# Optimization experiments

Measured on AMD Instinct MI355X. Metric: run time of the kernel, lower is better.

The kernel has to match this reference:

```python
import jax, jax.numpy as jnp
import numpy as np

B, S, D = 4, 4096, 2048
E, H, SPE = 64, 1024, 1
NUM_SLOTS = E * SPE
TEMP = 1.0


def setup_inputs() -> dict:
    key = jax.random.key(0)
    ks = jax.random.split(key, 6)
    x = jax.random.normal(ks[0], (B, S, D), dtype=jnp.float32)
    W_disp = jax.random.normal(ks[1], (NUM_SLOTS, D), dtype=jnp.float32) * 0.02
    # torch Linear default init ~ U(-1/sqrt(fan_in), 1/sqrt(fan_in))
    W1 = jax.random.uniform(ks[2], (E, H, D), jnp.float32, -1.0, 1.0) / np.sqrt(D)
    b1 = jax.random.uniform(ks[3], (E, H), jnp.float32, -1.0, 1.0) / np.sqrt(D)
    W2 = jax.random.uniform(ks[4], (E, D, H), jnp.float32, -1.0, 1.0) / np.sqrt(H)
    b2 = jax.random.uniform(ks[5], (E, D), jnp.float32, -1.0, 1.0) / np.sqrt(H)
    return {"x": x, "W_disp": W_disp, "W1": W1, "b1": b1, "W2": W2, "b2": b2}


def reference(x, W_disp, W1, b1, W2, b2):
    # eval mode: dropout inactive, no calibration, z_loss_weight=0
    Bb, Ss, Dd = x.shape
    xf = x.reshape(-1, Dd)                       # (T, D)
    logits = (xf @ W_disp.T) / TEMP              # (T, num_slots)
    dispatch = jax.nn.softmax(logits, axis=0)    # softmax over tokens (T > 1)
    combine = jax.nn.softmax(logits, axis=-1)    # softmax over slots
    slot_inputs = dispatch.T @ xf                # (num_slots, D)
    x_exp = slot_inputs.reshape(E, SPE, Dd)      # (E, S_per, D)
    h = jnp.einsum('esd,ehd->esh', x_exp, W1) + b1[:, None, :]
    h = jax.nn.gelu(h, approximate=False)        # torch F.gelu is exact (erf)
    out = jnp.einsum('esh,edh->esd', h, W2) + b2[:, None, :]
    slot_outputs = out.reshape(NUM_SLOTS, Dd)
    y = combine @ slot_outputs                   # (T, D)
    return y.reshape(Bb, Ss, Dd)
```

## Files before the change

kernel.cpp:

```cpp
#include <hip/hip_runtime.h>
#include <math.h>

#define T_TOK 16384
#define D_DIM 2048
#define NSLOT 64
#define H_DIM 1024
#define KSPLIT 8
#define KCH (D_DIM / KSPLIT)

__global__ __launch_bounds__(256) void k_logits(const float* __restrict__ x,
                                                const float* __restrict__ Wd,
                                                float* __restrict__ plog) {
    __shared__ float xs[256][32];
    __shared__ float ws[64][32];
    const int tid = threadIdx.x;
    const int tblk = blockIdx.x * 256;
    const int ks = blockIdx.y;
    const int koff = ks * KCH;
    const int tq = tid >> 3;
    const int sg = tid & 7;
    float acc[8][8] = {};

    for (int kc = 0; kc < KCH; kc += 32) {
        __syncthreads();
        #pragma unroll
        for (int ii = 0; ii < 8; ++ii) {
            int fi = tid + ii * 256;
            int t = fi >> 3, c = fi & 7;
            *(float4*)&xs[t][(c ^ (t & 7)) << 2] =
                *(const float4*)&x[(size_t)(tblk + t) * D_DIM + koff + kc + c * 4];
        }
        #pragma unroll
        for (int ii = 0; ii < 2; ++ii) {
            int fi = tid + ii * 256;
            int s = fi >> 3, c = fi & 7;
            *(float4*)&ws[s][(c ^ (s & 7)) << 2] =
                *(const float4*)&Wd[(size_t)s * D_DIM + koff + kc + c * 4];
        }
        __syncthreads();
        #pragma unroll
        for (int c = 0; c < 8; ++c) {
            float4 wv[8];
            #pragma unroll
            for (int j = 0; j < 8; ++j)
                wv[j] = *(const float4*)&ws[sg + 8 * j][(c ^ sg) << 2];
            #pragma unroll
            for (int i = 0; i < 8; ++i) {
                float4 xv = *(const float4*)&xs[tq + 32 * i][(c ^ (tq & 7)) << 2];
                #pragma unroll
                for (int j = 0; j < 8; ++j)
                    acc[i][j] += xv.x * wv[j].x + xv.y * wv[j].y +
                                 xv.z * wv[j].z + xv.w * wv[j].w;
            }
        }
    }
    #pragma unroll
    for (int i = 0; i < 8; ++i)
        #pragma unroll
        for (int j = 0; j < 8; ++j)
            plog[((size_t)ks * T_TOK + tblk + tq + 32 * i) * NSLOT + sg + 8 * j] =
                acc[i][j];
}

__global__ __launch_bounds__(256) void k_lsum(const float* __restrict__ plog,
                                              float* __restrict__ logits) {
    const size_t idx = ((size_t)blockIdx.x * 256 + threadIdx.x) * 4;
    float4 a = *(const float4*)&plog[idx];
    #pragma unroll
    for (int j = 1; j < KSPLIT; ++j) {
        float4 v = *(const float4*)&plog[(size_t)j * T_TOK * NSLOT + idx];
        a.x += v.x; a.y += v.y; a.z += v.z; a.w += v.w;
    }
    *(float4*)&logits[idx] = a;
}

__global__ __launch_bounds__(256) void k_cred1(const float* __restrict__ logits,
                                               float* __restrict__ pm,
                                               float* __restrict__ pz) {
    __shared__ float lm[256], lz[256];
    const int tid = threadIdx.x;
    const size_t base = (size_t)blockIdx.x * 256 * NSLOT;
    float m = -1e30f, z = 0.f;
    for (int i = 0; i < 64; ++i) {
        float v = logits[base + (size_t)i * 256 + tid];
        float nm = fmaxf(m, v);
        z = z * __expf(m - nm) + __expf(v - nm);
        m = nm;
    }
    lm[tid] = m; lz[tid] = z;
    __syncthreads();
    if (tid < 64) {
        float M = lm[tid], Z = lz[tid];
        #pragma unroll
        for (int i = 1; i < 4; ++i) {
            float m2 = lm[tid + i * 64], z2 = lz[tid + i * 64];
            float nm = fmaxf(M, m2);
            Z = Z * __expf(M - nm) + z2 * __expf(m2 - nm);
            M = nm;
        }
        pm[blockIdx.x * NSLOT + tid] = M;
        pz[blockIdx.x * NSLOT + tid] = Z;
    }
}

__global__ void k_cred2(const float* __restrict__ pm, const float* __restrict__ pz,
                        float* __restrict__ m_out, float* __restrict__ invZ_out) {
    const int s = threadIdx.x;
    float M = -1e30f, Z = 0.f;
    for (int i = 0; i < 64; ++i) {
        float m2 = pm[i * NSLOT + s], z2 = pz[i * NSLOT + s];
        float nm = fmaxf(M, m2);
        Z = Z * __expf(M - nm) + z2 * __expf(m2 - nm);
        M = nm;
    }
    m_out[s] = M;
    invZ_out[s] = 1.f / Z;
}

__global__ __launch_bounds__(256) void k_probs(const float* __restrict__ logits,
                                               const float* __restrict__ mS,
                                               const float* __restrict__ invZ,
                                               float* __restrict__ disp,
                                               float* __restrict__ comb) {
    const int wave = threadIdx.x >> 6, lane = threadIdx.x & 63;
    const int t = blockIdx.x * 4 + wave;
    float v = logits[(size_t)t * NSLOT + lane];
    float M = v;
    #pragma unroll
    for (int off = 32; off; off >>= 1) M = fmaxf(M, __shfl_xor(M, off));
    float e = __expf(v - M);
    float Z = e;
    #pragma unroll
    for (int off = 32; off; off >>= 1) Z += __shfl_xor(Z, off);
    comb[(size_t)t * NSLOT + lane] = e / Z;
    disp[(size_t)t * NSLOT + lane] = __expf(v - mS[lane]) * invZ[lane];
}

__global__ __launch_bounds__(256) void k_slot_inputs(const float* __restrict__ x,
        const float* __restrict__ disp, float* __restrict__ partial) {
    __shared__ float xs[32][256];
    __shared__ float pls[32][64];
    const int tid = threadIdx.x;
    const int d0 = blockIdx.x * 256;
    const int tc0 = blockIdx.y * 256;
    const int dg = tid & 31;
    const int sgq = tid >> 5;
    float4 acc0[8] = {}, acc1[8] = {};

    for (int sub = 0; sub < 8; ++sub) {
        const int t0 = tc0 + sub * 32;
        __syncthreads();
        #pragma unroll
        for (int ii = 0; ii < 8; ++ii) {
            int fi = tid + ii * 256;
            int r = fi >> 6, c4 = fi & 63;
            *(float4*)&xs[r][c4 * 4] =
                *(const float4*)&x[(size_t)(t0 + r) * D_DIM + d0 + c4 * 4];
        }
        #pragma unroll
        for (int ii = 0; ii < 2; ++ii) {
            int fi = tid + ii * 256;
            int r = fi >> 4, s4 = fi & 15;
            *(float4*)&pls[r][s4 * 4] =
                *(const float4*)&disp[(size_t)(t0 + r) * NSLOT + s4 * 4];
        }
        __syncthreads();
        for (int t = 0; t < 32; ++t) {
            float4 xv0 = *(const float4*)&xs[t][dg * 4];
            float4 xv1 = *(const float4*)&xs[t][128 + dg * 4];
            #pragma unroll
            for (int i = 0; i < 8; ++i) {
                float p = pls[t][sgq * 8 + i];
                acc0[i].x += p * xv0.x; acc0[i].y += p * xv0.y;
                acc0[i].z += p * xv0.z; acc0[i].w += p * xv0.w;
                acc1[i].x += p * xv1.x; acc1[i].y += p * xv1.y;
                acc1[i].z += p * xv1.z; acc1[i].w += p * xv1.w;
            }
        }
    }
    #pragma unroll
    for (int i = 0; i < 8; ++i) {
        int s = sgq * 8 + i;
        *(float4*)&partial[((size_t)blockIdx.y * NSLOT + s) * D_DIM + d0 + dg * 4] = acc0[i];
        *(float4*)&partial[((size_t)blockIdx.y * NSLOT + s) * D_DIM + d0 + 128 + dg * 4] = acc1[i];
    }
}

__global__ __launch_bounds__(256) void k_sred(const float* __restrict__ partial,
                                              float* __restrict__ slot_in) {
    const size_t idx = ((size_t)blockIdx.x * 256 + threadIdx.x) * 4;
    float4 a = {0.f, 0.f, 0.f, 0.f};
    for (int c = 0; c < 64; ++c) {
        float4 v = *(const float4*)&partial[(size_t)c * (NSLOT * D_DIM) + idx];
        a.x += v.x; a.y += v.y; a.z += v.z; a.w += v.w;
    }
    *(float4*)&slot_in[idx] = a;
}

__global__ __launch_bounds__(256) void k_mlp1(const float* __restrict__ W1,
                                              const float* __restrict__ b1,
                                              const float* __restrict__ slot_in,
                                              float* __restrict__ h) {
    const int wave = threadIdx.x >> 6, lane = threadIdx.x & 63;
    const int row = blockIdx.x * 4 + wave;
    const int e = row >> 10;
    const float* wr = W1 + (size_t)row * D_DIM;
    const float* xr = slot_in + (size_t)e * D_DIM;
    float acc = 0.f;
    #pragma unroll
    for (int i = 0; i < 8; ++i) {
        int k = (lane + i * 64) * 4;
        float4 w4 = *(const float4*)(wr + k);
        float4 x4 = *(const float4*)(xr + k);
        acc += w4.x * x4.x + w4.y * x4.y + w4.z * x4.z + w4.w * x4.w;
    }
    #pragma unroll
    for (int off = 32; off; off >>= 1) acc += __shfl_xor(acc, off);
    if (lane == 0) {
        float v = acc + b1[row];
        h[row] = 0.5f * v * (1.f + erff(v * 0.70710678118654752f));
    }
}

__global__ __launch_bounds__(256) void k_mlp2(const float* __restrict__ W2,
                                              const float* __restrict__ b2,
                                              const float* __restrict__ h,
                                              float* __restrict__ slot_out) {
    const int wave = threadIdx.x >> 6, lane = threadIdx.x & 63;
    const int row = blockIdx.x * 4 + wave;
    const int e = row >> 11;
    const float* wr = W2 + (size_t)row * H_DIM;
    const float* xr = h + (size_t)e * H_DIM;
    float acc = 0.f;
    #pragma unroll
    for (int i = 0; i < 4; ++i) {
        int k = (lane + i * 64) * 4;
        float4 w4 = *(const float4*)(wr + k);
        float4 x4 = *(const float4*)(xr + k);
        acc += w4.x * x4.x + w4.y * x4.y + w4.z * x4.z + w4.w * x4.w;
    }
    #pragma unroll
    for (int off = 32; off; off >>= 1) acc += __shfl_xor(acc, off);
    if (lane == 0) slot_out[row] = acc + b2[row];
}

__global__ __launch_bounds__(256) void k_combine(const float* __restrict__ comb,
                                                 const float* __restrict__ so,
                                                 float* __restrict__ y) {
    __shared__ float cl[128][68];
    __shared__ float sol[64][128];
    const int tid = threadIdx.x;
    const int d0 = blockIdx.x * 128;
    const int tb = blockIdx.y * 128;
    const int tq = tid >> 4;
    const int dgq = tid & 15;
    #pragma unroll
    for (int ii = 0; ii < 8; ++ii) {
        int fi = tid + ii * 256;
        int r = fi >> 4, s4 = fi & 15;
        *(float4*)&cl[r][s4 * 4] =
            *(const float4*)&comb[(size_t)(tb + r) * NSLOT + s4 * 4];
    }
    #pragma unroll
    for (int ii = 0; ii < 8; ++ii) {
        int fi = tid + ii * 256;
        int r = fi >> 5, c4 = fi & 31;
        *(float4*)&sol[r][c4 * 4] =
            *(const float4*)&so[(size_t)r * D_DIM + d0 + c4 * 4];
    }
    __syncthreads();
    float4 acc0[8] = {}, acc1[8] = {};
    for (int s = 0; s < 64; ++s) {
        float4 sv0 = *(const float4*)&sol[s][dgq * 4];
        float4 sv1 = *(const float4*)&sol[s][64 + dgq * 4];
        #pragma unroll
        for (int i = 0; i < 8; ++i) {
            float cv = cl[tq + 16 * i][s];
            acc0[i].x += cv * sv0.x; acc0[i].y += cv * sv0.y;
            acc0[i].z += cv * sv0.z; acc0[i].w += cv * sv0.w;
            acc1[i].x += cv * sv1.x; acc1[i].y += cv * sv1.y;
            acc1[i].z += cv * sv1.z; acc1[i].w += cv * sv1.w;
        }
    }
    #pragma unroll
    for (int i = 0; i < 8; ++i) {
        *(float4*)&y[(size_t)(tb + tq + 16 * i) * D_DIM + d0 + dgq * 4] = acc0[i];
        *(float4*)&y[(size_t)(tb + tq + 16 * i) * D_DIM + d0 + 64 + dgq * 4] = acc1[i];
    }
}

extern "C" void kernel_launch(void* const* d_in, const int* in_sizes, int n_in,
                              void* d_out, int out_size, void* d_ws, size_t ws_size,
                              hipStream_t stream) {
    const float* x  = (const float*)d_in[0];
    const float* Wd = (const float*)d_in[1];
    const float* W1 = (const float*)d_in[2];
    const float* b1 = (const float*)d_in[3];
    const float* W2 = (const float*)d_in[4];
    const float* b2 = (const float*)d_in[5];
    float* y = (float*)d_out;

    float* w = (float*)d_ws;
    float* plog    = w;
    float* logits  = plog + (size_t)KSPLIT * T_TOK * NSLOT;
    float* pm      = logits + (size_t)T_TOK * NSLOT;
    float* pz      = pm + 64 * NSLOT;
    float* mS      = pz + 64 * NSLOT;
    float* invZ    = mS + NSLOT;
    float* disp    = invZ + NSLOT;
    float* comb    = disp + (size_t)T_TOK * NSLOT;
    float* partial = comb + (size_t)T_TOK * NSLOT;
    float* slot_in = partial + (size_t)64 * NSLOT * D_DIM;
    float* h       = slot_in + (size_t)NSLOT * D_DIM;
    float* slot_out= h + (size_t)NSLOT * H_DIM;

    k_logits<<<dim3(T_TOK / 256, KSPLIT), 256, 0, stream>>>(x, Wd, plog);
    k_lsum<<<(T_TOK * NSLOT) / (4 * 256), 256, 0, stream>>>(plog, logits);
    k_cred1<<<64, 256, 0, stream>>>(logits, pm, pz);
    k_cred2<<<1, 64, 0, stream>>>(pm, pz, mS, invZ);
    k_probs<<<T_TOK / 4, 256, 0, stream>>>(logits, mS, invZ, disp, comb);
    k_slot_inputs<<<dim3(8, 64), 256, 0, stream>>>(x, disp, partial);
    k_sred<<<(NSLOT * D_DIM) / (4 * 256), 256, 0, stream>>>(partial, slot_in);
    k_mlp1<<<(NSLOT * H_DIM) / 4, 256, 0, stream>>>(W1, b1, slot_in, h);
    k_mlp2<<<(NSLOT * D_DIM) / 4, 256, 0, stream>>>(W2, b2, h, slot_out);
    k_combine<<<dim3(16, 128), 256, 0, stream>>>(comb, slot_out, y);
}
```

Measured before the change: 509.5 us.

## Fuse router front-end stages into one cooperative persistent kernel with grid syncs

Replaces seven front-end launches (logits GEMM, split-K sum, column softmax reductions, probs, slot-input GEMM, slot reduction) with a single cooperative kernel of 256 blocks separated by grid.sync. It halves KSPLIT, fuses the logit sum with per-block column stats and the row softmax, and computes dispatch probabilities on the fly instead of storing them. The aim is to cut launch gaps and intermediate global traffic. In exchange it runs far fewer blocks per stage (256 vs up to 512), pays for grid barriers, and serializes the final stat merge on one block.

```diff
diff --git a/kernel.cpp b/kernel.cpp
--- a/kernel.cpp
+++ b/kernel.cpp
@@ -1,200 +1,213 @@
 #include <hip/hip_runtime.h>
+#include <hip/hip_cooperative_groups.h>
 #include <math.h>
+
+namespace cg = cooperative_groups;
 
 #define T_TOK 16384
 #define D_DIM 2048
 #define NSLOT 64
 #define H_DIM 1024
-#define KSPLIT 8
-#define KCH (D_DIM / KSPLIT)
-
-__global__ __launch_bounds__(256) void k_logits(const float* __restrict__ x,
-                                                const float* __restrict__ Wd,
-                                                float* __restrict__ plog) {
-    __shared__ float xs[256][32];
-    __shared__ float ws[64][32];
+#define KSPLIT 4
+#define KCH 512
+#define NBLK 256
+
+__global__ __launch_bounds__(256, 2) void k_front(
+    const float* __restrict__ x, const float* __restrict__ Wd,
+    float* __restrict__ wsp)
+{
+    cg::grid_group grid = cg::this_grid();
     const int tid = threadIdx.x;
-    const int tblk = blockIdx.x * 256;
-    const int ks = blockIdx.y;
-    const int koff = ks * KCH;
-    const int tq = tid >> 3;
-    const int sg = tid & 7;
-    float acc[8][8] = {};
-
-    for (int kc = 0; kc < KCH; kc += 32) {
-        __syncthreads();
-        #pragma unroll
-        for (int ii = 0; ii < 8; ++ii) {
-            int fi = tid + ii * 256;
-            int t = fi >> 3, c = fi & 7;
-            *(float4*)&xs[t][(c ^ (t & 7)) << 2] =
-                *(const float4*)&x[(size_t)(tblk + t) * D_DIM + koff + kc + c * 4];
-        }
-        #pragma unroll
-        for (int ii = 0; ii < 2; ++ii) {
-            int fi = tid + ii * 256;
-            int s = fi >> 3, c = fi & 7;
-            *(float4*)&ws[s][(c ^ (s & 7)) << 2] =
-                *(const float4*)&Wd[(size_t)s * D_DIM + koff + kc + c * 4];
-        }
-        __syncthreads();
-        #pragma unroll
-        for (int c = 0; c < 8; ++c) {
-            float4 wv[8];
-            #pragma unroll
-            for (int j = 0; j < 8; ++j)
-                wv[j] = *(const float4*)&ws[sg + 8 * j][(c ^ sg) << 2];
-            #pragma unroll
-            for (int i = 0; i < 8; ++i) {
-                float4 xv = *(const float4*)&xs[tq + 32 * i][(c ^ (tq & 7)) << 2];
+    const int bid = blockIdx.x;
+
+    float* plog     = wsp;
+    float* logits   = plog + (size_t)KSPLIT * T_TOK * NSLOT;
+    float* comb     = logits + (size_t)T_TOK * NSLOT;
+    float* pm       = comb + (size_t)T_TOK * NSLOT;
+    float* pz       = pm + (size_t)NBLK * NSLOT;
+    float* mS       = pz + (size_t)NBLK * NSLOT;
+    float* invZ     = mS + NSLOT;
+    float* partial  = invZ + NSLOT;
+    float* slot_in  = partial + (size_t)32 * NSLOT * D_DIM;
+
+    __shared__ union {
+        struct { float xs[256][32]; float wsb[64][32]; } p1;
+        struct { float ls[64][66]; } p2;
+        struct { float lm[4][64]; float lz[4][64]; } p3;
+        struct { float xs[32][256]; float pls[32][64];
+                 float msh[64]; float zsh[64]; } p4;
+        struct { float4 red[256]; } p5;
+    } u;
+
+    {
+        const int tb = bid >> 2, ks = bid & 3;
+        const int tblk = tb * 256, koff = ks * KCH;
+        const int tq = tid >> 3, sg = tid & 7;
+        float acc[8][8] = {};
+        for (int kc = 0; kc < KCH; kc += 32) {
+            __syncthreads();
+            #pragma unroll
+            for (int ii = 0; ii < 8; ++ii) {
+                int fi = tid + ii * 256; int t = fi >> 3, c = fi & 7;
+                *(float4*)&u.p1.xs[t][(c ^ (t & 7)) << 2] =
+                    *(const float4*)&x[(size_t)(tblk + t) * D_DIM + koff + kc + c * 4];
+            }
+            #pragma unroll
+            for (int ii = 0; ii < 2; ++ii) {
+                int fi = tid + ii * 256; int s = fi >> 3, c = fi & 7;
+                *(float4*)&u.p1.wsb[s][(c ^ (s & 7)) << 2] =
+                    *(const float4*)&Wd[(size_t)s * D_DIM + koff + kc + c * 4];
+            }
+            __syncthreads();
+            #pragma unroll
+            for (int c = 0; c < 8; ++c) {
+                float4 wv[8];
                 #pragma unroll
                 for (int j = 0; j < 8; ++j)
-                    acc[i][j] += xv.x * wv[j].x + xv.y * wv[j].y +
-                                 xv.z * wv[j].z + xv.w * wv[j].w;
-            }
-        }
-    }
-    #pragma unroll
-    for (int i = 0; i < 8; ++i)
+                    wv[j] = *(const float4*)&u.p1.wsb[sg + 8 * j][(c ^ sg) << 2];
+                #pragma unroll
+                for (int i = 0; i < 8; ++i) {
+                    float4 xv = *(const float4*)&u.p1.xs[tq + 32 * i][(c ^ (tq & 7)) << 2];
+                    #pragma unroll
+                    for (int j = 0; j < 8; ++j)
+                        acc[i][j] += xv.x * wv[j].x + xv.y * wv[j].y +
+                                     xv.z * wv[j].z + xv.w * wv[j].w;
+                }
+            }
+        }
         #pragma unroll
-        for (int j = 0; j < 8; ++j)
-            plog[((size_t)ks * T_TOK + tblk + tq + 32 * i) * NSLOT + sg + 8 * j] =
-                acc[i][j];
-}
-
-__global__ __launch_bounds__(256) void k_lsum(const float* __restrict__ plog,
-                                              float* __restrict__ logits) {
-    const size_t idx = ((size_t)blockIdx.x * 256 + threadIdx.x) * 4;
-    float4 a = *(const float4*)&plog[idx];
-    #pragma unroll
-    for (int j = 1; j < KSPLIT; ++j) {
-        float4 v = *(const float4*)&plog[(size_t)j * T_TOK * NSLOT + idx];
-        a.x += v.x; a.y += v.y; a.z += v.z; a.w += v.w;
-    }
-    *(float4*)&logits[idx] = a;
-}
-
-__global__ __launch_bounds__(256) void k_cred1(const float* __restrict__ logits,
-                                               float* __restrict__ pm,
-                                               float* __restrict__ pz) {
-    __shared__ float lm[256], lz[256];
-    const int tid = threadIdx.x;
-    const size_t base = (size_t)blockIdx.x * 256 * NSLOT;
-    float m = -1e30f, z = 0.f;
-    for (int i = 0; i < 64; ++i) {
-        float v = logits[base + (size_t)i * 256 + tid];
-        float nm = fmaxf(m, v);
-        z = z * __expf(m - nm) + __expf(v - nm);
-        m = nm;
-    }
-    lm[tid] = m; lz[tid] = z;
-    __syncthreads();
-    if (tid < 64) {
-        float M = lm[tid], Z = lz[tid];
+        for (int i = 0; i < 8; ++i)
+            #pragma unroll
+            for (int j = 0; j < 8; ++j)
+                plog[((size_t)ks * T_TOK + tblk + tq + 32 * i) * NSLOT + sg + 8 * j] =
+                    acc[i][j];
+    }
+    grid.sync();
+
+    {
+        const int j0 = bid * 64;
         #pragma unroll
-        for (int i = 1; i < 4; ++i) {
-            float m2 = lm[tid + i * 64], z2 = lz[tid + i * 64];
-            float nm = fmaxf(M, m2);
-            Z = Z * __expf(M - nm) + z2 * __expf(m2 - nm);
-            M = nm;
-        }
-        pm[blockIdx.x * NSLOT + tid] = M;
-        pz[blockIdx.x * NSLOT + tid] = Z;
-    }
-}
-
-__global__ void k_cred2(const float* __restrict__ pm, const float* __restrict__ pz,
-                        float* __restrict__ m_out, float* __restrict__ invZ_out) {
-    const int s = threadIdx.x;
-    float M = -1e30f, Z = 0.f;
-    for (int i = 0; i < 64; ++i) {
-        float m2 = pm[i * NSLOT + s], z2 = pz[i * NSLOT + s];
-        float nm = fmaxf(M, m2);
-        Z = Z * __expf(M - nm) + z2 * __expf(m2 - nm);
-        M = nm;
-    }
-    m_out[s] = M;
-    invZ_out[s] = 1.f / Z;
-}
-
-__global__ __launch_bounds__(256) void k_probs(const float* __restrict__ logits,
-                                               const float* __restrict__ mS,
-                                               const float* __restrict__ invZ,
-                                               float* __restrict__ disp,
-                                               float* __restrict__ comb) {
-    const int wave = threadIdx.x >> 6, lane = threadIdx.x & 63;
-    const int t = blockIdx.x * 4 + wave;
-    float v = logits[(size_t)t * NSLOT + lane];
-    float M = v;
-    #pragma unroll
-    for (int off = 32; off; off >>= 1) M = fmaxf(M, __shfl_xor(M, off));
-    float e = __expf(v - M);
-    float Z = e;
-    #pragma unroll
-    for (int off = 32; off; off >>= 1) Z += __shfl_xor(Z, off);
-    comb[(size_t)t * NSLOT + lane] = e / Z;
-    disp[(size_t)t * NSLOT + lane] = __expf(v - mS[lane]) * invZ[lane];
-}
-
-__global__ __launch_bounds__(256) void k_slot_inputs(const float* __restrict__ x,
-        const float* __restrict__ disp, float* __restrict__ partial) {
-    __shared__ float xs[32][256];
-    __shared__ float pls[32][64];
-    const int tid = threadIdx.x;
-    const int d0 = blockIdx.x * 256;
-    const int tc0 = blockIdx.y * 256;
-    const int dg = tid & 31;
-    const int sgq = tid >> 5;
-    float4 acc0[8] = {}, acc1[8] = {};
-
-    for (int sub = 0; sub < 8; ++sub) {
-        const int t0 = tc0 + sub * 32;
+        for (int ii = 0; ii < 16; ++ii) {
+            int fi = tid + ii * 256; int r = fi >> 6, s = fi & 63;
+            float a = 0.f;
+            #pragma unroll
+            for (int ks = 0; ks < KSPLIT; ++ks)
+                a += plog[((size_t)ks * T_TOK + j0 + r) * NSLOT + s];
+            logits[(size_t)(j0 + r) * NSLOT + s] = a;
+            u.p2.ls[r][s] = a;
+        }
         __syncthreads();
+        if (tid < 64) {
+            float m = -1e30f, z = 0.f;
+            for (int r = 0; r < 64; ++r) {
+                float v = u.p2.ls[r][tid];
+                float nm = fmaxf(m, v);
+                z = z * __expf(m - nm) + __expf(v - nm);
+                m = nm;
+            }
+            pm[(size_t)bid * NSLOT + tid] = m;
+            pz[(size_t)bid * NSLOT + tid] = z;
+        } else if (tid < 128) {
+            const int r = tid - 64;
+            float M = -1e30f;
+            for (int s = 0; s < 64; ++s) M = fmaxf(M, u.p2.ls[r][s]);
+            float Z = 0.f;
+            for (int s = 0; s < 64; ++s) Z += __expf(u.p2.ls[r][s] - M);
+            float rz = 1.f / Z;
+            for (int s = 0; s < 64; ++s)
+                comb[(size_t)(j0 + r) * NSLOT + s] = __expf(u.p2.ls[r][s] - M) * rz;
+        }
+    }
+    grid.sync();
+
+    if (bid == 0) {
+        const int part = tid >> 6, s = tid & 63;
+        float m = -1e30f, z = 0.f;
+        for (int c = part * 64; c < part * 64 + 64; ++c) {
+            float m2 = pm[(size_t)c * NSLOT + s], z2 = pz[(size_t)c * NSLOT + s];
+            float nm = fmaxf(m, m2);
+            z = z * __expf(m - nm) + z2 * __expf(m2 - nm);
+            m = nm;
+        }
+        u.p3.lm[part][s] = m; u.p3.lz[part][s] = z;
+        __syncthreads();
+        if (tid < 64) {
+            float M = u.p3.lm[0][tid], Z = u.p3.lz[0][tid];
+            #pragma unroll
+            for (int p = 1; p < 4; ++p) {
+                float m2 = u.p3.lm[p][tid], z2 = u.p3.lz[p][tid];
+                float nm = fmaxf(M, m2);
+                Z = Z * __expf(M - nm) + z2 * __expf(m2 - nm);
+                M = nm;
+            }
+            mS[tid] = M; invZ[tid] = 1.f / Z;
+        }
+    }
+    grid.sync();
+
+    {
+        const int dt = bid & 7, tc = bid >> 3;
+        const int d0 = dt * 256, tc0 = tc * 512;
+        if (tid < 64) { u.p4.msh[tid] = mS[tid]; u.p4.zsh[tid] = invZ[tid]; }
+        const int dg = tid & 31, sgq = tid >> 5;
+        float4 acc0[8] = {}, acc1[8] = {};
+        for (int sub = 0; sub < 16; ++sub) {
+            const int t0 = tc0 + sub * 32;
+            __syncthreads();
+            #pragma unroll
+            for (int ii = 0; ii < 8; ++ii) {
+                int fi = tid + ii * 256; int r = fi >> 6, c4 = fi & 63;
+                *(float4*)&u.p4.xs[r][c4 * 4] =
+                    *(const float4*)&x[(size_t)(t0 + r) * D_DIM + d0 + c4 * 4];
+            }
+            #pragma unroll
+            for (int ii = 0; ii < 8; ++ii) {
+                int fi = tid + ii * 256; int r = fi >> 6, s = fi & 63;
+                u.p4.pls[r][s] =
+                    __expf(logits[(size_t)(t0 + r) * NSLOT + s] - u.p4.msh[s]) * u.p4.zsh[s];
+            }
+            __syncthreads();
+            for (int t = 0; t < 32; ++t) {
+                float4 xv0 = *(const float4*)&u.p4.xs[t][dg * 4];
+                float4 xv1 = *(const float4*)&u.p4.xs[t][128 + dg * 4];
+                #pragma unroll
+                for (int i = 0; i < 8; ++i) {
+                    float p = u.p4.pls[t][sgq * 8 + i];
+                    acc0[i].x += p * xv0.x; acc0[i].y += p * xv0.y;
+                    acc0[i].z += p * xv0.z; acc0[i].w += p * xv0.w;
+                    acc1[i].x += p * xv1.x; acc1[i].y += p * xv1.y;
+                    acc1[i].z += p * xv1.z; acc1[i].w += p * xv1.w;
+                }
+            }
+        }
         #pragma unroll
-        for (int ii = 0; ii < 8; ++ii) {
-            int fi = tid + ii * 256;
-            int r = fi >> 6, c4 = fi & 63;
-            *(float4*)&xs[r][c4 * 4] =
-                *(const float4*)&x[(size_t)(t0 + r) * D_DIM + d0 + c4 * 4];
-        }
-        #pragma unroll
-        for (int ii = 0; ii < 2; ++ii) {
-            int fi = tid + ii * 256;
-            int r = fi >> 4, s4 = fi & 15;
-            *(float4*)&pls[r][s4 * 4] =
-                *(const float4*)&disp[(size_t)(t0 + r) * NSLOT + s4 * 4];
-        }
+        for (int i = 0; i < 8; ++i) {
+            int s = sgq * 8 + i;
+            *(float4*)&partial[((size_t)tc * NSLOT + s) * D_DIM + d0 + dg * 4] = acc0[i];
+            *(float4*)&partial[((size_t)tc * NSLOT + s) * D_DIM + d0 + 128 + dg * 4] = acc1[i];
+        }
+    }
+    grid.sync();
+
+    {
+        const float4* partial4 = (const float4*)partial;
+        float4* slot_in4 = (float4*)slot_in;
+        const int o = bid * 128 + (tid & 127);
+        const int part = tid >> 7;
+        float4 a = {0.f, 0.f, 0.f, 0.f};
+        for (int c = part * 16; c < part * 16 + 16; ++c) {
+            float4 v = partial4[(size_t)c * (NSLOT * D_DIM / 4) + o];
+            a.x += v.x; a.y += v.y; a.z += v.z; a.w += v.w;
+        }
+        u.p5.red[tid] = a;
         __syncthreads();
-        for (int t = 0; t < 32; ++t) {
-            float4 xv0 = *(const float4*)&xs[t][dg * 4];
-            float4 xv1 = *(const float4*)&xs[t][128 + dg * 4];
-            #pragma unroll
-            for (int i = 0; i < 8; ++i) {
-                float p = pls[t][sgq * 8 + i];
-                acc0[i].x += p * xv0.x; acc0[i].y += p * xv0.y;
-                acc0[i].z += p * xv0.z; acc0[i].w += p * xv0.w;
-                acc1[i].x += p * xv1.x; acc1[i].y += p * xv1.y;
-                acc1[i].z += p * xv1.z; acc1[i].w += p * xv1.w;
-            }
-        }
-    }
-    #pragma unroll
-    for (int i = 0; i < 8; ++i) {
-        int s = sgq * 8 + i;
-        *(float4*)&partial[((size_t)blockIdx.y * NSLOT + s) * D_DIM + d0 + dg * 4] = acc0[i];
-        *(float4*)&partial[((size_t)blockIdx.y * NSLOT + s) * D_DIM + d0 + 128 + dg * 4] = acc1[i];
-    }
-}
-
-__global__ __launch_bounds__(256) void k_sred(const float* __restrict__ partial,
-                                              float* __restrict__ slot_in) {
-    const size_t idx = ((size_t)blockIdx.x * 256 + threadIdx.x) * 4;
-    float4 a = {0.f, 0.f, 0.f, 0.f};
-    for (int c = 0; c < 64; ++c) {
-        float4 v = *(const float4*)&partial[(size_t)c * (NSLOT * D_DIM) + idx];
-        a.x += v.x; a.y += v.y; a.z += v.z; a.w += v.w;
-    }
-    *(float4*)&slot_in[idx] = a;
+        if (tid < 128) {
+            float4 b = u.p5.red[tid];
+            float4 v = u.p5.red[tid + 128];
+            b.x += v.x; b.y += v.y; b.z += v.z; b.w += v.w;
+            slot_in4[o] = b;
+        }
+    }
 }
 
 __global__ __launch_bounds__(256) void k_mlp1(const float* __restrict__ W1,
@@ -298,29 +311,25 @@
     const float* b1 = (const float*)d_in[3];
     const float* W2 = (const float*)d_in[4];
     const float* b2 = (const float*)d_in[5];
-    float* y = (float*)d_out;
-
-    float* w = (float*)d_ws;
-    float* plog    = w;
-    float* logits  = plog + (size_t)KSPLIT * T_TOK * NSLOT;
-    float* pm      = logits + (size_t)T_TOK * NSLOT;
-    float* pz      = pm + 64 * NSLOT;
-    float* mS      = pz + 64 * NSLOT;
-    float* invZ    = mS + NSLOT;
-    float* disp    = invZ + NSLOT;
-    float* comb    = disp + (size_t)T_TOK * NSLOT;
-    float* partial = comb + (size_t)T_TOK * NSLOT;
-    float* slot_in = partial + (size_t)64 * NSLOT * D_DIM;
-    float* h       = slot_in + (size_t)NSLOT * D_DIM;
-    float* slot_out= h + (size_t)NSLOT * H_DIM;
-
-    k_logits<<<dim3(T_TOK / 256, KSPLIT), 256, 0, stream>>>(x, Wd, plog);
-    k_lsum<<<(T_TOK * NSLOT) / (4 * 256), 256, 0, stream>>>(plog, logits);
-    k_cred1<<<64, 256, 0, stream>>>(logits, pm, pz);
-    k_cred2<<<1, 64, 0, stream>>>(pm, pz, mS, invZ);
-    k_probs<<<T_TOK / 4, 256, 0, stream>>>(logits, mS, invZ, disp, comb);
-    k_slot_inputs<<<dim3(8, 64), 256, 0, stream>>>(x, disp, partial);
-    k_sred<<<(NSLOT * D_DIM) / (4 * 256), 256, 0, stream>>>(partial, slot_in);
+    float* y   = (float*)d_out;
+    float* wsp = (float*)d_ws;
+
+    float* plog     = wsp;
+    float* logits   = plog + (size_t)KSPLIT * T_TOK * NSLOT;
+    float* comb     = logits + (size_t)T_TOK * NSLOT;
+    float* pm       = comb + (size_t)T_TOK * NSLOT;
+    float* pz       = pm + (size_t)NBLK * NSLOT;
+    float* mS       = pz + (size_t)NBLK * NSLOT;
+    float* invZ     = mS + NSLOT;
+    float* partial  = invZ + NSLOT;
+    float* slot_in  = partial + (size_t)32 * NSLOT * D_DIM;
+    float* h        = slot_in + (size_t)NSLOT * D_DIM;
+    float* slot_out = h + (size_t)NSLOT * H_DIM;
+    (void)logits; (void)pm; (void)pz; (void)mS; (void)invZ; (void)partial;
+
+    void* args[] = {(void*)&x, (void*)&Wd, (void*)&wsp};
+    hipLaunchCooperativeKernel((void*)k_front, dim3(NBLK), dim3(256), args, 0, stream);
+
     k_mlp1<<<(NSLOT * H_DIM) / 4, 256, 0, stream>>>(W1, b1, slot_in, h);
     k_mlp2<<<(NSLOT * D_DIM) / 4, 256, 0, stream>>>(W2, b2, h, slot_out);
     k_combine<<<dim3(16, 128), 256, 0, stream>>>(comb, slot_out, y);
```

Measured after the change: 1.321 ms. 2.59x slower.

## Fuse split-K logit sum with exp and defer softmax normalization to consumers

Applied to the files above, without the earlier changes.

Folds the split-K logit summation, the exponentiation and the per-slot column-sum partials into one kernel. It replaces the separate max/sum reductions and the probability kernel with a single exp(logit) buffer. Dispatch normalization (1/Z per slot) moves into the slot reduction, and combine normalization (per-token row sum) is computed inside the combine kernel. This removes several launches and full T×64 intermediate reads and writes. The logits GEMM tile is also halved to 128 tokens per block. It drops max-subtraction, so it relies on logits staying small enough not to overflow exp, and the fused reduction kernel runs with only 64 blocks.

```diff
diff --git a/kernel.cpp b/kernel.cpp
--- a/kernel.cpp
+++ b/kernel.cpp
@@ -6,34 +6,32 @@
 #define NSLOT 64
 #define H_DIM 1024
 #define KSPLIT 8
-#define KCH (D_DIM / KSPLIT)
+#define KCH 256
+#define TBLK 128
 
 __global__ __launch_bounds__(256) void k_logits(const float* __restrict__ x,
                                                 const float* __restrict__ Wd,
                                                 float* __restrict__ plog) {
-    __shared__ float xs[256][32];
+    __shared__ float xs[128][32];
     __shared__ float ws[64][32];
     const int tid = threadIdx.x;
-    const int tblk = blockIdx.x * 256;
-    const int ks = blockIdx.y;
-    const int koff = ks * KCH;
+    const int tblk = blockIdx.x * TBLK;
+    const int koff = blockIdx.y * KCH;
     const int tq = tid >> 3;
     const int sg = tid & 7;
-    float acc[8][8] = {};
+    float acc[4][8] = {};
 
     for (int kc = 0; kc < KCH; kc += 32) {
         __syncthreads();
         #pragma unroll
-        for (int ii = 0; ii < 8; ++ii) {
-            int fi = tid + ii * 256;
-            int t = fi >> 3, c = fi & 7;
+        for (int ii = 0; ii < 4; ++ii) {
+            int fi = tid + ii * 256; int t = fi >> 3, c = fi & 7;
             *(float4*)&xs[t][(c ^ (t & 7)) << 2] =
                 *(const float4*)&x[(size_t)(tblk + t) * D_DIM + koff + kc + c * 4];
         }
         #pragma unroll
         for (int ii = 0; ii < 2; ++ii) {
-            int fi = tid + ii * 256;
-            int s = fi >> 3, c = fi & 7;
+            int fi = tid + ii * 256; int s = fi >> 3, c = fi & 7;
             *(float4*)&ws[s][(c ^ (s & 7)) << 2] =
                 *(const float4*)&Wd[(size_t)s * D_DIM + koff + kc + c * 4];
         }
@@ -45,7 +43,7 @@
             for (int j = 0; j < 8; ++j)
                 wv[j] = *(const float4*)&ws[sg + 8 * j][(c ^ sg) << 2];
             #pragma unroll
-            for (int i = 0; i < 8; ++i) {
+            for (int i = 0; i < 4; ++i) {
                 float4 xv = *(const float4*)&xs[tq + 32 * i][(c ^ (tq & 7)) << 2];
                 #pragma unroll
                 for (int j = 0; j < 8; ++j)
@@ -54,97 +52,53 @@
             }
         }
     }
-    #pragma unroll
-    for (int i = 0; i < 8; ++i)
+    const size_t ksbase = (size_t)blockIdx.y * T_TOK;
+    #pragma unroll
+    for (int i = 0; i < 4; ++i)
         #pragma unroll
         for (int j = 0; j < 8; ++j)
-            plog[((size_t)ks * T_TOK + tblk + tq + 32 * i) * NSLOT + sg + 8 * j] =
-                acc[i][j];
+            plog[(ksbase + tblk + tq + 32 * i) * NSLOT + sg + 8 * j] = acc[i][j];
 }
 
 __global__ __launch_bounds__(256) void k_lsum(const float* __restrict__ plog,
-                                              float* __restrict__ logits) {
-    const size_t idx = ((size_t)blockIdx.x * 256 + threadIdx.x) * 4;
-    float4 a = *(const float4*)&plog[idx];
-    #pragma unroll
-    for (int j = 1; j < KSPLIT; ++j) {
-        float4 v = *(const float4*)&plog[(size_t)j * T_TOK * NSLOT + idx];
-        a.x += v.x; a.y += v.y; a.z += v.z; a.w += v.w;
-    }
-    *(float4*)&logits[idx] = a;
-}
-
-__global__ __launch_bounds__(256) void k_cred1(const float* __restrict__ logits,
-                                               float* __restrict__ pm,
-                                               float* __restrict__ pz) {
-    __shared__ float lm[256], lz[256];
-    const int tid = threadIdx.x;
-    const size_t base = (size_t)blockIdx.x * 256 * NSLOT;
-    float m = -1e30f, z = 0.f;
+                                              float* __restrict__ elog,
+                                              float* __restrict__ pz) {
+    __shared__ float zsh[4][64];
+    const int tid = threadIdx.x;
+    const int s = tid & 63, rq = tid >> 6;
+    const int j0 = blockIdx.x * 256;
+    float zacc = 0.f;
     for (int i = 0; i < 64; ++i) {
-        float v = logits[base + (size_t)i * 256 + tid];
-        float nm = fmaxf(m, v);
-        z = z * __expf(m - nm) + __expf(v - nm);
-        m = nm;
-    }
-    lm[tid] = m; lz[tid] = z;
+        int r = j0 + rq * 64 + i;
+        float v = 0.f;
+        #pragma unroll
+        for (int ks = 0; ks < KSPLIT; ++ks)
+            v += plog[((size_t)ks * T_TOK + r) * NSLOT + s];
+        float e = __expf(v);
+        elog[(size_t)r * NSLOT + s] = e;
+        zacc += e;
+    }
+    zsh[rq][s] = zacc;
     __syncthreads();
-    if (tid < 64) {
-        float M = lm[tid], Z = lz[tid];
-        #pragma unroll
-        for (int i = 1; i < 4; ++i) {
-            float m2 = lm[tid + i * 64], z2 = lz[tid + i * 64];
-            float nm = fmaxf(M, m2);
-            Z = Z * __expf(M - nm) + z2 * __expf(m2 - nm);
-            M = nm;
-        }
-        pm[blockIdx.x * NSLOT + tid] = M;
-        pz[blockIdx.x * NSLOT + tid] = Z;
-    }
-}
-
-__global__ void k_cred2(const float* __restrict__ pm, const float* __restrict__ pz,
-                        float* __restrict__ m_out, float* __restrict__ invZ_out) {
-    const int s = threadIdx.x;
-    float M = -1e30f, Z = 0.f;
-    for (int i = 0; i < 64; ++i) {
-        float m2 = pm[i * NSLOT + s], z2 = pz[i * NSLOT + s];
-        float nm = fmaxf(M, m2);
-        Z = Z * __expf(M - nm) + z2 * __expf(m2 - nm);
-        M = nm;
-    }
-    m_out[s] = M;
-    invZ_out[s] = 1.f / Z;
-}
-
-__global__ __launch_bounds__(256) void k_probs(const float* __restrict__ logits,
-                                               const float* __restrict__ mS,
-                                               const float* __restrict__ invZ,
-                                               float* __restrict__ disp,
-                                               float* __restrict__ comb) {
-    const int wave = threadIdx.x >> 6, lane = threadIdx.x & 63;
-    const int t = blockIdx.x * 4 + wave;
-    float v = logits[(size_t)t * NSLOT + lane];
-    float M = v;
-    #pragma unroll
-    for (int off = 32; off; off >>= 1) M = fmaxf(M, __shfl_xor(M, off));
-    float e = __expf(v - M);
-    float Z = e;
-    #pragma unroll
-    for (int off = 32; off; off >>= 1) Z += __shfl_xor(Z, off);
-    comb[(size_t)t * NSLOT + lane] = e / Z;
-    disp[(size_t)t * NSLOT + lane] = __expf(v - mS[lane]) * invZ[lane];
-}
-
-__global__ __launch_bounds__(256) void k_slot_inputs(const float* __restrict__ x,
-        const float* __restrict__ disp, float* __restrict__ partial) {
+    if (tid < 64)
+        pz[(size_t)blockIdx.x * NSLOT + tid] =
+            zsh[0][tid] + zsh[1][tid] + zsh[2][tid] + zsh[3][tid];
+}
+
+__global__ void k_zred(const float* __restrict__ pz, float* __restrict__ invZ) {
+    float z = 0.f;
+    for (int b = 0; b < 64; ++b) z += pz[b * NSLOT + threadIdx.x];
+    invZ[threadIdx.x] = 1.f / z;
+}
+
+__global__ __launch_bounds__(256) void k_slot(const float* __restrict__ x,
+        const float* __restrict__ elog, float* __restrict__ partial) {
     __shared__ float xs[32][256];
     __shared__ float pls[32][64];
     const int tid = threadIdx.x;
     const int d0 = blockIdx.x * 256;
     const int tc0 = blockIdx.y * 256;
-    const int dg = tid & 31;
-    const int sgq = tid >> 5;
+    const int dg = tid & 31, sgq = tid >> 5;
     float4 acc0[8] = {}, acc1[8] = {};
 
     for (int sub = 0; sub < 8; ++sub) {
@@ -152,17 +106,15 @@
         __syncthreads();
         #pragma unroll
         for (int ii = 0; ii < 8; ++ii) {
-            int fi = tid + ii * 256;
-            int r = fi >> 6, c4 = fi & 63;
+            int fi = tid + ii * 256; int r = fi >> 6, c4 = fi & 63;
             *(float4*)&xs[r][c4 * 4] =
                 *(const float4*)&x[(size_t)(t0 + r) * D_DIM + d0 + c4 * 4];
         }
         #pragma unroll
         for (int ii = 0; ii < 2; ++ii) {
-            int fi = tid + ii * 256;
-            int r = fi >> 4, s4 = fi & 15;
+            int fi = tid + ii * 256; int r = fi >> 4, s4 = fi & 15;
             *(float4*)&pls[r][s4 * 4] =
-                *(const float4*)&disp[(size_t)(t0 + r) * NSLOT + s4 * 4];
+                *(const float4*)&elog[(size_t)(t0 + r) * NSLOT + s4 * 4];
         }
         __syncthreads();
         for (int t = 0; t < 32; ++t) {
@@ -187,14 +139,17 @@
 }
 
 __global__ __launch_bounds__(256) void k_sred(const float* __restrict__ partial,
+                                              const float* __restrict__ invZ,
                                               float* __restrict__ slot_in) {
-    const size_t idx = ((size_t)blockIdx.x * 256 + threadIdx.x) * 4;
+    const size_t idx = (size_t)blockIdx.x * 256 + threadIdx.x;
+    const float iz = invZ[idx >> 9];
     float4 a = {0.f, 0.f, 0.f, 0.f};
     for (int c = 0; c < 64; ++c) {
-        float4 v = *(const float4*)&partial[(size_t)c * (NSLOT * D_DIM) + idx];
+        float4 v = ((const float4*)partial)[(size_t)c * (NSLOT * D_DIM / 4) + idx];
         a.x += v.x; a.y += v.y; a.z += v.z; a.w += v.w;
     }
-    *(float4*)&slot_in[idx] = a;
+    a.x *= iz; a.y *= iz; a.z *= iz; a.w *= iz;
+    ((float4*)slot_in)[idx] = a;
 }
 
 __global__ __launch_bounds__(256) void k_mlp1(const float* __restrict__ W1,
@@ -244,11 +199,12 @@
     if (lane == 0) slot_out[row] = acc + b2[row];
 }
 
-__global__ __launch_bounds__(256) void k_combine(const float* __restrict__ comb,
+__global__ __launch_bounds__(256) void k_combine(const float* __restrict__ elog,
                                                  const float* __restrict__ so,
                                                  float* __restrict__ y) {
     __shared__ float cl[128][68];
     __shared__ float sol[64][128];
+    __shared__ float rinv[128];
     const int tid = threadIdx.x;
     const int d0 = blockIdx.x * 128;
     const int tb = blockIdx.y * 128;
@@ -256,17 +212,25 @@
     const int dgq = tid & 15;
     #pragma unroll
     for (int ii = 0; ii < 8; ++ii) {
-        int fi = tid + ii * 256;
-        int r = fi >> 4, s4 = fi & 15;
+        int fi = tid + ii * 256; int r = fi >> 4, s4 = fi & 15;
         *(float4*)&cl[r][s4 * 4] =
-            *(const float4*)&comb[(size_t)(tb + r) * NSLOT + s4 * 4];
+            *(const float4*)&elog[(size_t)(tb + r) * NSLOT + s4 * 4];
     }
     #pragma unroll
     for (int ii = 0; ii < 8; ++ii) {
-        int fi = tid + ii * 256;
-        int r = fi >> 5, c4 = fi & 31;
+        int fi = tid + ii * 256; int r = fi >> 5, c4 = fi & 31;
         *(float4*)&sol[r][c4 * 4] =
             *(const float4*)&so[(size_t)r * D_DIM + d0 + c4 * 4];
+    }
+    __syncthreads();
+    if (tid < 128) {
+        float zs = 0.f;
+        #pragma unroll
+        for (int q = 0; q < 16; ++q) {
+            float4 v = *(const float4*)&cl[tid][q * 4];
+            zs += v.x + v.y + v.z + v.w;
+        }
+        rinv[tid] = 1.f / zs;
     }
     __syncthreads();
     float4 acc0[8] = {}, acc1[8] = {};
@@ -284,6 +248,9 @@
     }
     #pragma unroll
     for (int i = 0; i < 8; ++i) {
+        float rz = rinv[tq + 16 * i];
+        acc0[i].x *= rz; acc0[i].y *= rz; acc0[i].z *= rz; acc0[i].w *= rz;
+        acc1[i].x *= rz; acc1[i].y *= rz; acc1[i].z *= rz; acc1[i].w *= rz;
         *(float4*)&y[(size_t)(tb + tq + 16 * i) * D_DIM + d0 + dgq * 4] = acc0[i];
         *(float4*)&y[(size_t)(tb + tq + 16 * i) * D_DIM + d0 + 64 + dgq * 4] = acc1[i];
     }
@@ -301,27 +268,21 @@
     float* y = (float*)d_out;
 
     float* w = (float*)d_ws;
-    float* plog    = w;
-    float* logits  = plog + (size_t)KSPLIT * T_TOK * NSLOT;
-    float* pm      = logits + (size_t)T_TOK * NSLOT;
-    float* pz      = pm + 64 * NSLOT;
-    float* mS      = pz + 64 * NSLOT;
-    float* invZ    = mS + NSLOT;
-    float* disp    = invZ + NSLOT;
-    float* comb    = disp + (size_t)T_TOK * NSLOT;
-    float* partial = comb + (size_t)T_TOK * NSLOT;
-    float* slot_in = partial + (size_t)64 * NSLOT * D_DIM;
-    float* h       = slot_in + (size_t)NSLOT * D_DIM;
-    float* slot_out= h + (size_t)NSLOT * H_DIM;
-
-    k_logits<<<dim3(T_TOK / 256, KSPLIT), 256, 0, stream>>>(x, Wd, plog);
-    k_lsum<<<(T_TOK * NSLOT) / (4 * 256), 256, 0, stream>>>(plog, logits);
-    k_cred1<<<64, 256, 0, stream>>>(logits, pm, pz);
-    k_cred2<<<1, 64, 0, stream>>>(pm, pz, mS, invZ);
-    k_probs<<<T_TOK / 4, 256, 0, stream>>>(logits, mS, invZ, disp, comb);
-    k_slot_inputs<<<dim3(8, 64), 256, 0, stream>>>(x, disp, partial);
-    k_sred<<<(NSLOT * D_DIM) / (4 * 256), 256, 0, stream>>>(partial, slot_in);
+    float* plog     = w;
+    float* elog     = plog + (size_t)KSPLIT * T_TOK * NSLOT;
+    float* pz       = elog + (size_t)T_TOK * NSLOT;
+    float* invZ     = pz + 64 * NSLOT;
+    float* partial  = invZ + NSLOT;
+    float* slot_in  = partial + (size_t)64 * NSLOT * D_DIM;
+    float* h        = slot_in + (size_t)NSLOT * D_DIM;
+    float* slot_out = h + (size_t)NSLOT * H_DIM;
+
+    k_logits<<<dim3(T_TOK / TBLK, KSPLIT), 256, 0, stream>>>(x, Wd, plog);
+    k_lsum<<<64, 256, 0, stream>>>(plog, elog, pz);
+    k_zred<<<1, 64, 0, stream>>>(pz, invZ);
+    k_slot<<<dim3(8, 64), 256, 0, stream>>>(x, elog, partial);
+    k_sred<<<128, 256, 0, stream>>>(partial, invZ, slot_in);
     k_mlp1<<<(NSLOT * H_DIM) / 4, 256, 0, stream>>>(W1, b1, slot_in, h);
     k_mlp2<<<(NSLOT * D_DIM) / 4, 256, 0, stream>>>(W2, b2, h, slot_out);
-    k_combine<<<dim3(16, 128), 256, 0, stream>>>(comb, slot_out, y);
-}
+    k_combine<<<dim3(16, 128), 256, 0, stream>>>(elog, slot_out, y);
+}
```

After: 470.2 us. 7.7% less time.
